# Optimization experiments

Measured on AMD Instinct MI355X. Metric: run time of the kernel, lower is better.

## Reference

```python
import jax, jax.numpy as jnp
import numpy as np

B, C_IN, C_OUT, N, MODES, TEMB = 16, 64, 64, 16384, 2048, 512


def setup_inputs() -> dict:
    key = jax.random.key(0)
    k1, k2, k3, k4, k5 = jax.random.split(key, 5)
    scale = 1.0 / (C_IN * C_OUT)
    return {
        "x": jax.random.normal(k1, (B, C_IN, N), dtype=jnp.float32),
        "temb": jax.random.normal(k2, (B, TEMB), dtype=jnp.float32),
        "wr": jax.random.normal(k3, (C_IN, C_OUT, MODES), dtype=jnp.float32) * scale,
        "wi": jax.random.normal(k4, (C_IN, C_OUT, MODES), dtype=jnp.float32) * scale,
        "dense_w": jax.random.normal(k5, (C_IN, TEMB), dtype=jnp.float32) * (1.0 / np.sqrt(TEMB)),
        "dense_b": jnp.zeros((C_IN,), dtype=jnp.float32),
    }


def reference(x, temb, wr, wi, dense_w, dense_b):
    # x: [B, C_in, N] real signal; spectral conv in Fourier space (FNO)
    b, c_in, n = x.shape
    modes = wr.shape[-1]
    x_ft = jnp.fft.rfft(x, axis=-1)  # [B, C_in, N//2+1] complex
    # temb injection: Dense_0(act(temb))[:, :, None], act = SiLU (DDPM-style)
    t = jax.nn.silu(temb) @ dense_w.T + dense_b  # [B, C_in]
    xm = x_ft[..., :modes] + t[:, :, None].astype(x_ft.dtype)
    w = wr + 1j * wi  # [C_in, C_out, modes]
    # contract_dense eq for order-3 input: 'abc,bdc->adc'
    out_m = jnp.einsum("bim,iom->bom", xm, w)  # [B, C_out, modes]
    c_out = w.shape[1]
    out_ft = jnp.zeros((b, c_out, n // 2 + 1), dtype=out_m.dtype)
    out_ft = out_ft.at[..., :modes].set(out_m)
    return jnp.fft.irfft(out_ft, n=n, axis=-1)  # [B, C_out, N]
```

## Files before the change

kernel.cpp:

```cpp
#include <hip/hip_runtime.h>
#include <math.h>

#define NB    16
#define CIN   64
#define COUT  64
#define NN    16384
#define HH    8192
#define MODES 2048
#define TEMBD 512

__device__ __forceinline__ int swz(int e) { return e ^ ((e >> 5) & 31); }
__device__ __forceinline__ int rev13(int x) { return (int)(__brev((unsigned)x) >> 19); }

__global__ void init_tw_k(float2* __restrict__ tw8, float2* __restrict__ tw16) {
  int j = blockIdx.x * blockDim.x + threadIdx.x;
  if (j < 4096) {
    double a = (2.0 * 3.14159265358979323846 / 8192.0) * (double)j;
    tw8[j] = make_float2((float)cos(a), (float)sin(a));
  }
  if (j < 2048) {
    double a = (2.0 * 3.14159265358979323846 / 16384.0) * (double)j;
    tw16[j] = make_float2((float)cos(a), (float)sin(a));
  }
}

template<int J, int S, int LH_HI>
__device__ __forceinline__ void pass_dif(float* zr, float* zi, int pbase,
                                         const float2* __restrict__ tw) {
  int lh = LH_HI;
#pragma unroll
  for (int half = J / 2; half >= 1; half >>= 1, --lh) {
#pragma unroll
    for (int blk = 0; blk < J; blk += 2 * half) {
#pragma unroll
      for (int q = 0; q < half; ++q) {
        const int j0 = blk + q, j1 = j0 + half;
        const float2 w = tw[(pbase + q * S) << (12 - lh)];
        const float ur = zr[j0], ui = zi[j0];
        const float vr = zr[j1], vi = zi[j1];
        zr[j0] = ur + vr; zi[j0] = ui + vi;
        const float br = ur - vr, bi = ui - vi;
        zr[j1] = br * w.x + bi * w.y;
        zi[j1] = bi * w.x - br * w.y;
      }
    }
  }
}

template<int J, int S, int LH_LO>
__device__ __forceinline__ void pass_dit(float* zr, float* zi, int pbase,
                                         const float2* __restrict__ tw) {
  int lh = LH_LO;
#pragma unroll
  for (int half = 1; half <= J / 2; half <<= 1, ++lh) {
#pragma unroll
    for (int blk = 0; blk < J; blk += 2 * half) {
#pragma unroll
      for (int q = 0; q < half; ++q) {
        const int j0 = blk + q, j1 = j0 + half;
        const float2 w = tw[(pbase + q * S) << (12 - lh)];
        const float vr = zr[j1], vi = zi[j1];
        const float tr = vr * w.x - vi * w.y;
        const float ti = vr * w.y + vi * w.x;
        const float ur = zr[j0], ui = zi[j0];
        zr[j0] = ur + tr; zi[j0] = ui + ti;
        zr[j1] = ur - tr; zi[j1] = ui - ti;
      }
    }
  }
}

__global__ __launch_bounds__(256) void fwd_fft_k(
    const float* __restrict__ x, const float* __restrict__ temb,
    const float* __restrict__ dw, const float* __restrict__ db,
    const float2* __restrict__ tw8, const float2* __restrict__ tw16,
    float2* __restrict__ xm)
{
  __shared__ float re[HH];
  __shared__ float im[HH];
  const int row = blockIdx.x;
  const int b = row >> 6, ci = row & 63;
  const int tid = threadIdx.x;

  float part = 0.f;
  {
    const float* tb = temb + b * TEMBD;
    const float* wrow = dw + ci * TEMBD;
    for (int j = tid; j < TEMBD; j += 256) {
      float v = tb[j];
      part += v * wrow[j] / (1.f + __expf(-v));
    }
    for (int off = 32; off > 0; off >>= 1) part += __shfl_down(part, off, 64);
    if ((tid & 63) == 0) re[tid >> 6] = part;
  }
  __syncthreads();
  const float tval = re[0] + re[1] + re[2] + re[3] + db[ci];
  __syncthreads();

  float zr[32], zi[32];

  const float2* xr = (const float2*)(x + (size_t)row * NN);
#pragma unroll
  for (int g = 0; g < 2; ++g) {
    const int i0 = tid + g * 256;
#pragma unroll
    for (int j = 0; j < 16; ++j) {
      float2 v = xr[i0 + j * 512];
      zr[g * 16 + j] = v.x; zi[g * 16 + j] = v.y;
    }
  }
#pragma unroll
  for (int g = 0; g < 2; ++g) {
    const int i0 = tid + g * 256;
    pass_dif<16, 512, 12>(zr + g * 16, zi + g * 16, i0, tw8);
#pragma unroll
    for (int j = 0; j < 16; ++j) {
      const int e = swz(i0 + j * 512);
      re[e] = zr[g * 16 + j]; im[e] = zi[g * 16 + j];
    }
  }
  __syncthreads();

  {
    const int r = tid & 31;
#pragma unroll
    for (int g = 0; g < 2; ++g) {
      const int base = ((tid >> 5) + g * 8) * 512 + r;
#pragma unroll
      for (int j = 0; j < 16; ++j) {
        const int e = swz(base + j * 32);
        zr[g * 16 + j] = re[e]; zi[g * 16 + j] = im[e];
      }
      pass_dif<16, 32, 8>(zr + g * 16, zi + g * 16, r, tw8);
#pragma unroll
      for (int j = 0; j < 16; ++j) {
        const int e = swz(base + j * 32);
        re[e] = zr[g * 16 + j]; im[e] = zi[g * 16 + j];
      }
    }
  }
  __syncthreads();

  {
    const int base = tid * 32;
#pragma unroll
    for (int j = 0; j < 32; ++j) {
      const int e = swz(base + j);
      zr[j] = re[e]; zi[j] = im[e];
    }
    pass_dif<32, 1, 4>(zr, zi, 0, tw8);
#pragma unroll
    for (int j = 0; j < 32; ++j) {
      const int e = swz(base + j);
      re[e] = zr[j]; im[e] = zi[j];
    }
  }
  __syncthreads();

  float2* xrow = xm + (size_t)row * MODES;
  for (int k = tid; k < MODES; k += 256) {
    const int ka = swz(rev13(k));
    const int kb = swz(rev13((HH - k) & (HH - 1)));
    float Ar = re[ka], Ai = im[ka];
    float Br = re[kb], Bi = -im[kb];
    float Sr = 0.5f * (Ar + Br), Si = 0.5f * (Ai + Bi);
    float Dr = 0.5f * (Ar - Br), Di = 0.5f * (Ai - Bi);
    float2 wv = tw16[k];
    float c = wv.x, s = wv.y;
    float Xr = Sr - s * Dr + c * Di;
    float Xi = Si - s * Di - c * Dr;
    xrow[k] = make_float2(Xr + tval, Xi);
  }
}

__global__ __launch_bounds__(256) void spec_mul_k(
    const float2* __restrict__ xm, const float* __restrict__ wr,
    const float* __restrict__ wi, float2* __restrict__ om)
{
  const int m = blockIdx.x * 64 + (threadIdx.x & 63);
  const int o = blockIdx.y * 4 + (threadIdx.x >> 6);
  const int b0 = blockIdx.z * 4;
  float2 acc[4];
#pragma unroll
  for (int b = 0; b < 4; ++b) acc[b] = make_float2(0.f, 0.f);
  for (int i = 0; i < CIN; ++i) {
    const size_t widx = ((size_t)(i * COUT + o)) * MODES + m;
    const float wrv = wr[widx];
    const float wiv = wi[widx];
#pragma unroll
    for (int b = 0; b < 4; ++b) {
      float2 xv = xm[((size_t)((b0 + b) * CIN + i)) * MODES + m];
      acc[b].x += xv.x * wrv - xv.y * wiv;
      acc[b].y += xv.x * wiv + xv.y * wrv;
    }
  }
#pragma unroll
  for (int b = 0; b < 4; ++b)
    om[((size_t)((b0 + b) * COUT + o)) * MODES + m] = acc[b];
}

__global__ __launch_bounds__(256) void inv_fft_k(
    const float2* __restrict__ om, const float2* __restrict__ tw8,
    const float2* __restrict__ tw16, float* __restrict__ out)
{
  __shared__ float re[HH];
  __shared__ float im[HH];
  const int row = blockIdx.x;
  const int tid = threadIdx.x;

  for (int q = tid; q < HH; q += 256) { re[q] = 0.f; im[q] = 0.f; }
  __syncthreads();

  const float2* grow = om + (size_t)row * MODES;
  for (int k = tid; k < MODES; k += 256) {
    float2 g = grow[k];
    if (k == 0) {
      float v = 0.5f * g.x;
      re[0] = v; im[0] = v;
    } else {
      float2 wv = tw16[k];
      float Pr = 0.5f * g.x, Pi = 0.5f * g.y;
      float c = wv.x, s = wv.y;
      float sr = -(c * Pi + s * Pr);
      float si =  (c * Pr - s * Pi);
      int ka = swz(rev13(k));
      int kb = swz(rev13(HH - k));
      re[ka] = Pr + sr; im[ka] = Pi + si;
      re[kb] = Pr - sr; im[kb] = -(Pi - si);
    }
  }
  __syncthreads();

  float zr[32], zi[32];

  {
    const int base = tid * 32;
#pragma unroll
    for (int j = 0; j < 32; ++j) {
      const int e = swz(base + j);
      zr[j] = re[e]; zi[j] = im[e];
    }
    pass_dit<32, 1, 0>(zr, zi, 0, tw8);
#pragma unroll
    for (int j = 0; j < 32; ++j) {
      const int e = swz(base + j);
      re[e] = zr[j]; im[e] = zi[j];
    }
  }
  __syncthreads();

  {
    const int r = tid & 31;
#pragma unroll
    for (int g = 0; g < 2; ++g) {
      const int base = ((tid >> 5) + g * 8) * 512 + r;
#pragma unroll
      for (int j = 0; j < 16; ++j) {
        const int e = swz(base + j * 32);
        zr[g * 16 + j] = re[e]; zi[g * 16 + j] = im[e];
      }
      pass_dit<16, 32, 5>(zr + g * 16, zi + g * 16, r, tw8);
#pragma unroll
      for (int j = 0; j < 16; ++j) {
        const int e = swz(base + j * 32);
        re[e] = zr[g * 16 + j]; im[e] = zi[g * 16 + j];
      }
    }
  }
  __syncthreads();

  {
    float2* orow = (float2*)(out + (size_t)row * NN);
    const float sc = 1.0f / 8192.0f;
#pragma unroll
    for (int g = 0; g < 2; ++g) {
      const int i0 = tid + g * 256;
#pragma unroll
      for (int j = 0; j < 16; ++j) {
        const int e = swz(i0 + j * 512);
        zr[g * 16 + j] = re[e]; zi[g * 16 + j] = im[e];
      }
      pass_dit<16, 512, 9>(zr + g * 16, zi + g * 16, i0, tw8);
#pragma unroll
      for (int j = 0; j < 16; ++j) {
        orow[i0 + j * 512] = make_float2(zr[g * 16 + j] * sc, zi[g * 16 + j] * sc);
      }
    }
  }
}

extern "C" void kernel_launch(void* const* d_in, const int* in_sizes, int n_in,
                              void* d_out, int out_size, void* d_ws, size_t ws_size,
                              hipStream_t stream) {
  const float* x    = (const float*)d_in[0];
  const float* temb = (const float*)d_in[1];
  const float* wr   = (const float*)d_in[2];
  const float* wi   = (const float*)d_in[3];
  const float* dw   = (const float*)d_in[4];
  const float* db   = (const float*)d_in[5];
  float* out = (float*)d_out;

  char* ws = (char*)d_ws;
  float2* tw8  = (float2*)ws;
  float2* tw16 = (float2*)(ws + 32768);
  float2* xm   = (float2*)(ws + 65536);
  float2* om   = (float2*)(ws + 65536 + (size_t)16777216);

  hipLaunchKernelGGL(init_tw_k, dim3(16), dim3(256), 0, stream, tw8, tw16);
  hipLaunchKernelGGL(fwd_fft_k, dim3(NB * CIN), dim3(256), 0, stream,
                     x, temb, dw, db, tw8, tw16, xm);
  hipLaunchKernelGGL(spec_mul_k, dim3(MODES / 64, COUT / 4, NB / 4), dim3(256), 0, stream,
                     xm, wr, wi, om);
  hipLaunchKernelGGL(inv_fft_k, dim3(NB * COUT), dim3(256), 0, stream,
                     om, tw8, tw16, out);
}
```

Measured before the change: 292.8 us.

## Tile spectral multiply through LDS with async global-to-LDS loads across all batches

Measured after the change: 250.3 us. 14.5% less time.

```diff
diff --git a/kernel.cpp b/kernel.cpp
--- a/kernel.cpp
+++ b/kernel.cpp
@@ -11,6 +11,12 @@
 
 __device__ __forceinline__ int swz(int e) { return e ^ ((e >> 5) & 31); }
 __device__ __forceinline__ int rev13(int x) { return (int)(__brev((unsigned)x) >> 19); }
+
+__device__ __forceinline__ void gl_lds16(const void* gsrc, void* lds) {
+  __builtin_amdgcn_global_load_lds(
+      (const __attribute__((address_space(1))) void*)gsrc,
+      (__attribute__((address_space(3))) void*)lds, 16, 0, 0);
+}
 
 __global__ void init_tw_k(float2* __restrict__ tw8, float2* __restrict__ tw16) {
   int j = blockIdx.x * blockDim.x + threadIdx.x;
@@ -173,30 +179,70 @@
   }
 }
 
-__global__ __launch_bounds__(256) void spec_mul_k(
+__global__ __launch_bounds__(512) void spec_mul_k(
     const float2* __restrict__ xm, const float* __restrict__ wr,
     const float* __restrict__ wi, float2* __restrict__ om)
 {
-  const int m = blockIdx.x * 64 + (threadIdx.x & 63);
-  const int o = blockIdx.y * 4 + (threadIdx.x >> 6);
-  const int b0 = blockIdx.z * 4;
-  float2 acc[4];
-#pragma unroll
-  for (int b = 0; b < 4; ++b) acc[b] = make_float2(0.f, 0.f);
-  for (int i = 0; i < CIN; ++i) {
-    const size_t widx = ((size_t)(i * COUT + o)) * MODES + m;
-    const float wrv = wr[widx];
-    const float wiv = wi[widx];
-#pragma unroll
-    for (int b = 0; b < 4; ++b) {
-      float2 xv = xm[((size_t)((b0 + b) * CIN + i)) * MODES + m];
-      acc[b].x += xv.x * wrv - xv.y * wiv;
-      acc[b].y += xv.x * wiv + xv.y * wrv;
-    }
-  }
-#pragma unroll
-  for (int b = 0; b < 4; ++b)
-    om[((size_t)((b0 + b) * COUT + o)) * MODES + m] = acc[b];
+  __shared__ float2 xs[16 * 8 * 32];
+  __shared__ float4 wsh[8 * 8 * 16];
+
+  const int tid = threadIdx.x;
+  const int mp = tid & 15;
+  const int od = (tid >> 4) & 7;
+  const int h  = tid >> 7;
+  const int wv = tid >> 6;
+  const int ln = tid & 63;
+
+  const int m0 = blockIdx.x * 32;
+  const int o0 = blockIdx.y * 8;
+  const int m2 = m0 + mp * 2;
+
+  float4 acc[4];
+#pragma unroll
+  for (int j = 0; j < 4; ++j) acc[j] = make_float4(0.f, 0.f, 0.f, 0.f);
+
+  for (int ic = 0; ic < 8; ++ic) {
+#pragma unroll
+    for (int t = 0; t < 4; ++t) {
+      const int r = wv * 16 + t * 4 + (ln >> 4);
+      const int b = r >> 3, il = r & 7;
+      const float2* src =
+          xm + ((size_t)(b * CIN + ic * 8 + il)) * MODES + m0 + (ln & 15) * 2;
+      gl_lds16((const void*)src, (void*)((char*)xs + (wv * 16 + t * 4) * 256));
+    }
+#pragma unroll
+    for (int t = 0; t < 2; ++t) {
+      const int e = tid + t * 512;
+      const int il = e >> 7, eo = (e >> 4) & 7, emp = e & 15;
+      const size_t wb =
+          ((size_t)((ic * 8 + il) * COUT + o0 + eo)) * MODES + m0 + emp * 2;
+      const float2 a = *(const float2*)(wr + wb);
+      const float2 c = *(const float2*)(wi + wb);
+      wsh[e] = make_float4(a.x, a.y, c.x, c.y);
+    }
+    __syncthreads();
+
+#pragma unroll
+    for (int il = 0; il < 8; ++il) {
+      const float4 w4 = wsh[(il * 8 + od) * 16 + mp];
+#pragma unroll
+      for (int j = 0; j < 4; ++j) {
+        const float4 xv = *(const float4*)&xs[((h * 4 + j) * 8 + il) * 32 + mp * 2];
+        acc[j].x += xv.x * w4.x - xv.y * w4.z;
+        acc[j].y += xv.x * w4.z + xv.y * w4.x;
+        acc[j].z += xv.z * w4.y - xv.w * w4.w;
+        acc[j].w += xv.z * w4.w + xv.w * w4.y;
+      }
+    }
+    __syncthreads();
+  }
+
+  const int o = o0 + od;
+#pragma unroll
+  for (int j = 0; j < 4; ++j) {
+    const int b = h * 4 + j;
+    *(float4*)(om + ((size_t)(b * COUT + o)) * MODES + m2) = acc[j];
+  }
 }
 
 __global__ __launch_bounds__(256) void inv_fft_k(
@@ -309,7 +355,7 @@
   hipLaunchKernelGGL(init_tw_k, dim3(16), dim3(256), 0, stream, tw8, tw16);
   hipLaunchKernelGGL(fwd_fft_k, dim3(NB * CIN), dim3(256), 0, stream,
                      x, temb, dw, db, tw8, tw16, xm);
-  hipLaunchKernelGGL(spec_mul_k, dim3(MODES / 64, COUT / 4, NB / 4), dim3(256), 0, stream,
+  hipLaunchKernelGGL(spec_mul_k, dim3(MODES / 32, COUT / 8), dim3(512), 0, stream,
                      xm, wr, wi, om);
   hipLaunchKernelGGL(inv_fft_k, dim3(NB * COUT), dim3(256), 0, stream,
                      om, tw8, tw16, out);
```

## Tile spectral multiply with LDS double buffering and skip unused FFT stores

Applied to the files above, without the earlier changes.

Result: faster. 264.6 us (-9.6%).

```diff
diff --git a/kernel.cpp b/kernel.cpp
--- a/kernel.cpp
+++ b/kernel.cpp
@@ -11,6 +11,12 @@
 
 __device__ __forceinline__ int swz(int e) { return e ^ ((e >> 5) & 31); }
 __device__ __forceinline__ int rev13(int x) { return (int)(__brev((unsigned)x) >> 19); }
+
+__device__ __forceinline__ void gl_lds16(const void* gsrc, void* lds) {
+  __builtin_amdgcn_global_load_lds(
+      (const __attribute__((address_space(1))) void*)gsrc,
+      (__attribute__((address_space(3))) void*)lds, 16, 0, 0);
+}
 
 __global__ void init_tw_k(float2* __restrict__ tw8, float2* __restrict__ tw16) {
   int j = blockIdx.x * blockDim.x + threadIdx.x;
@@ -151,6 +157,7 @@
     pass_dif<32, 1, 4>(zr, zi, 0, tw8);
 #pragma unroll
     for (int j = 0; j < 32; ++j) {
+      if ((j & 3) == 1 || (j & 3) == 2) continue;
       const int e = swz(base + j);
       re[e] = zr[j]; im[e] = zi[j];
     }
@@ -177,26 +184,105 @@
     const float2* __restrict__ xm, const float* __restrict__ wr,
     const float* __restrict__ wi, float2* __restrict__ om)
 {
-  const int m = blockIdx.x * 64 + (threadIdx.x & 63);
-  const int o = blockIdx.y * 4 + (threadIdx.x >> 6);
-  const int b0 = blockIdx.z * 4;
-  float2 acc[4];
-#pragma unroll
-  for (int b = 0; b < 4; ++b) acc[b] = make_float2(0.f, 0.f);
-  for (int i = 0; i < CIN; ++i) {
-    const size_t widx = ((size_t)(i * COUT + o)) * MODES + m;
-    const float wrv = wr[widx];
-    const float wiv = wi[widx];
-#pragma unroll
-    for (int b = 0; b < 4; ++b) {
-      float2 xv = xm[((size_t)((b0 + b) * CIN + i)) * MODES + m];
-      acc[b].x += xv.x * wrv - xv.y * wiv;
-      acc[b].y += xv.x * wiv + xv.y * wrv;
-    }
-  }
-#pragma unroll
-  for (int b = 0; b < 4; ++b)
-    om[((size_t)((b0 + b) * COUT + o)) * MODES + m] = acc[b];
+  __shared__ float2 xs[2][128 * 16];
+  __shared__ float4 wsh[2][1024];
+
+  const int tid = threadIdx.x;
+  const int mp = tid & 7;
+  const int og = (tid >> 3) & 7;
+  const int h  = tid >> 6;
+  const int ln = tid & 63;
+
+  const int m0 = blockIdx.x * 16;
+  const int o0 = blockIdx.y * 16;
+
+  float4 acc[4][2];
+#pragma unroll
+  for (int j = 0; j < 4; ++j) {
+    acc[j][0] = make_float4(0.f, 0.f, 0.f, 0.f);
+    acc[j][1] = make_float4(0.f, 0.f, 0.f, 0.f);
+  }
+
+  float2 wrv[4], wiv[4];
+
+#define STAGE_X(ic, buf)                                                      \
+  {                                                                           \
+    _Pragma("unroll")                                                         \
+    for (int t = 0; t < 4; ++t) {                                             \
+      const int r = h * 32 + t * 8 + (ln >> 3);                               \
+      const int b = r >> 3, il = r & 7;                                       \
+      const float2* src =                                                     \
+          xm + ((size_t)(b * CIN + (ic) * 8 + il)) * MODES + m0 + (ln & 7) * 2;\
+      gl_lds16((const void*)src, (void*)((char*)&xs[buf][0] + (h * 4 + t) * 1024)); \
+    }                                                                         \
+  }
+
+#define W_LOAD(ic)                                                            \
+  {                                                                           \
+    _Pragma("unroll")                                                         \
+    for (int t = 0; t < 4; ++t) {                                             \
+      const int e = tid + t * 256;                                            \
+      const int il = e >> 7, oo = (e >> 6) & 1, g2 = (e >> 3) & 7, ep = e & 7;\
+      const int o = g2 * 2 + oo;                                              \
+      const size_t wb =                                                       \
+          ((size_t)(((ic) * 8 + il) * COUT + o0 + o)) * MODES + m0 + ep * 2;  \
+      wrv[t] = *(const float2*)(wr + wb);                                     \
+      wiv[t] = *(const float2*)(wi + wb);                                     \
+    }                                                                         \
+  }
+
+#define W_WRITE(buf)                                                          \
+  {                                                                           \
+    _Pragma("unroll")                                                         \
+    for (int t = 0; t < 4; ++t)                                               \
+      wsh[buf][tid + t * 256] =                                               \
+          make_float4(wrv[t].x, wrv[t].y, wiv[t].x, wiv[t].y);                \
+  }
+
+  STAGE_X(0, 0);
+  W_LOAD(0);
+  W_WRITE(0);
+  __syncthreads();
+
+  for (int ic = 0; ic < 8; ++ic) {
+    const int buf = ic & 1;
+    if (ic < 7) {
+      STAGE_X(ic + 1, buf ^ 1);
+      W_LOAD(ic + 1);
+    }
+#pragma unroll
+    for (int il = 0; il < 8; ++il) {
+      const float4 wA = wsh[buf][il * 128 + og * 8 + mp];
+      const float4 wB = wsh[buf][il * 128 + 64 + og * 8 + mp];
+#pragma unroll
+      for (int j = 0; j < 4; ++j) {
+        const float4 xv = *(const float4*)&xs[buf][((h * 4 + j) * 8 + il) * 16 + mp * 2];
+        acc[j][0].x += xv.x * wA.x - xv.y * wA.z;
+        acc[j][0].y += xv.x * wA.z + xv.y * wA.x;
+        acc[j][0].z += xv.z * wA.y - xv.w * wA.w;
+        acc[j][0].w += xv.z * wA.w + xv.w * wA.y;
+        acc[j][1].x += xv.x * wB.x - xv.y * wB.z;
+        acc[j][1].y += xv.x * wB.z + xv.y * wB.x;
+        acc[j][1].z += xv.z * wB.y - xv.w * wB.w;
+        acc[j][1].w += xv.z * wB.w + xv.w * wB.y;
+      }
+    }
+    if (ic < 7) W_WRITE(buf ^ 1);
+    __syncthreads();
+  }
+
+#pragma unroll
+  for (int j = 0; j < 4; ++j) {
+    const int b = h * 4 + j;
+#pragma unroll
+    for (int oo = 0; oo < 2; ++oo) {
+      const int o = o0 + og * 2 + oo;
+      *(float4*)(om + ((size_t)(b * COUT + o)) * MODES + m0 + mp * 2) = acc[j][oo];
+    }
+  }
+#undef STAGE_X
+#undef W_LOAD
+#undef W_WRITE
 }
 
 __global__ __launch_bounds__(256) void inv_fft_k(
@@ -309,7 +395,7 @@
   hipLaunchKernelGGL(init_tw_k, dim3(16), dim3(256), 0, stream, tw8, tw16);
   hipLaunchKernelGGL(fwd_fft_k, dim3(NB * CIN), dim3(256), 0, stream,
                      x, temb, dw, db, tw8, tw16, xm);
-  hipLaunchKernelGGL(spec_mul_k, dim3(MODES / 64, COUT / 4, NB / 4), dim3(256), 0, stream,
+  hipLaunchKernelGGL(spec_mul_k, dim3(MODES / 16, COUT / 16), dim3(256), 0, stream,
                      xm, wr, wi, om);
   hipLaunchKernelGGL(inv_fft_k, dim3(NB * COUT), dim3(256), 0, stream,
                      om, tw8, tw16, out);
```
